# Kernel tuning notes

Hardware: AMD Instinct MI355X
Metric: run time of the kernel (lower is better)

Reference implementation:

```python
import jax, jax.numpy as jnp
import numpy as np

N_NODES = 100000
N_EDGES = 3200000
H, D = 3, 12  # heads, per-head dim; H*D == node_hidden_dim == 36
NEG_SLOPE = 0.2


def setup_inputs() -> dict:
    key = jax.random.key(0)
    ks = jax.random.split(key, 11)
    s = 0.1
    return {
        "node_features": jax.random.normal(ks[0], (N_NODES, 36), jnp.float32),
        "src": jax.random.randint(ks[1], (N_EDGES,), 0, N_NODES),
        "dst": jax.random.randint(ks[2], (N_EDGES,), 0, N_NODES),
        "lin0_w": jax.random.normal(ks[3], (36, 36), jnp.float32) * s,
        "lin0_b": jax.random.normal(ks[4], (36,), jnp.float32) * s,
        "fc_w": jax.random.normal(ks[5], (3, 36, 36), jnp.float32) * s,
        "attn_l": jax.random.normal(ks[6], (3, H, D), jnp.float32) * s,
        "attn_r": jax.random.normal(ks[7], (3, H, D), jnp.float32) * s,
        "gat_bias": jax.random.normal(ks[8], (3, 36), jnp.float32) * s,
        "out_w": jax.random.normal(ks[9], (36, 36), jnp.float32) * s,
        "out_b": jax.random.normal(ks[10], (36,), jnp.float32) * s,
    }


def _gat_layer(h, src, dst, fc_w, a_l, a_r, bias):
    n = h.shape[0]
    feat = (h @ fc_w).reshape(n, H, D)                      # (N,H,D)
    el = jnp.sum(feat * a_l, axis=-1)                       # (N,H)
    er = jnp.sum(feat * a_r, axis=-1)                       # (N,H)
    e = el[src] + er[dst]                                   # (E,H)
    e = jnp.where(e >= 0, e, NEG_SLOPE * e)                 # leaky_relu(0.2)
    # edge softmax over incoming edges of each dst node (numerically stable)
    m = jax.ops.segment_max(e, dst, num_segments=n)         # (N,H)
    m = jnp.where(jnp.isfinite(m), m, 0.0)                  # zero-degree guard
    ee = jnp.exp(e - m[dst])                                # (E,H)
    denom = jax.ops.segment_sum(ee, dst, num_segments=n)    # (N,H)
    alpha = ee / jnp.maximum(denom[dst], 1e-9)              # (E,H)
    msg = feat[src] * alpha[:, :, None]                     # (E,H,D)
    rst = jax.ops.segment_sum(msg, dst, num_segments=n)     # (N,H,D)
    # residual (Identity since in_feats == H*D) + bias, then ELU
    rst = rst + h.reshape(n, H, D) + bias.reshape(1, H, D)
    return jax.nn.elu(rst).reshape(n, H * D)


def reference(node_features, src, dst, lin0_w, lin0_b, fc_w, attn_l, attn_r, gat_bias, out_w, out_b):
    h = node_features @ lin0_w + lin0_b
    for l in range(3):
        h = _gat_layer(h, src, dst, fc_w[l], attn_l[l], attn_r[l], gat_bias[l])
    return h @ out_w + out_b
```

## Files before the change

kernel.cpp:

```cpp
#include <hip/hip_runtime.h>
#include <math.h>

#define HID 36
#define NH 3
#define HD 12
#define PROW 64
#define BSHIFT 13
#define NBUCK 13
#define PSHIFT 8
#define PCHUNK 8192
#define CSRCAP 4096
#define NSTEP 8

typedef _Float16 f16;


__global__ void hist2_kernel(const int* __restrict__ dst, int* __restrict__ M,
                             int E, int C, int np) {
    __shared__ int h[512];
    int t = threadIdx.x;
    int c = blockIdx.x;
    for (int i = t; i < 512; i += blockDim.x) h[i] = 0;
    __syncthreads();
    int i0 = c * PCHUNK;
    int i1 = min(i0 + PCHUNK, E);
    for (int i = i0 + t; i < i1; i += blockDim.x)
        atomicAdd(&h[dst[i] >> PSHIFT], 1);
    __syncthreads();
    for (int b = t; b < np; b += blockDim.x)
        M[(size_t)b * C + c] = h[b];
}

__global__ void base_scan_kernel(const int* __restrict__ M, int* __restrict__ BaseT,
                                 int* __restrict__ T, int C, int np) {
    __shared__ int tmp[512];
    int b = blockIdx.x;
    int t = threadIdx.x;
    int v = (t < C) ? M[(size_t)b * C + t] : 0;
    tmp[t] = v;
    __syncthreads();
    for (int ofs = 1; ofs < 512; ofs <<= 1) {
        int x = 0;
        if (t >= ofs) x = tmp[t - ofs];
        __syncthreads();
        tmp[t] += x;
        __syncthreads();
    }
    if (t < C) BaseT[(size_t)t * 512 + b] = tmp[t] - v;
    if (t == 511) T[b] = tmp[511];
}

__global__ void scan_small_kernel(const int* __restrict__ T, int* __restrict__ poff, int np) {
    __shared__ int tmp[512];
    int t = threadIdx.x;
    int v = (t < np) ? T[t] : 0;
    tmp[t] = v;
    __syncthreads();
    for (int ofs = 1; ofs < 512; ofs <<= 1) {
        int x = 0;
        if (t >= ofs) x = tmp[t - ofs];
        __syncthreads();
        tmp[t] += x;
        __syncthreads();
    }
    int excl = tmp[t] - v;
    if (t < np) poff[t] = excl;
    if (t == np - 1) poff[np] = excl + v;
}

__global__ void part_scatter_kernel(const int* __restrict__ src, const int* __restrict__ dst,
                                    const int* __restrict__ BaseT, const int* __restrict__ poff,
                                    int* __restrict__ part, int E, int np) {
    __shared__ int h[512];
    __shared__ int base[512];
    int t = threadIdx.x;
    int c = blockIdx.x;
    for (int i = t; i < 512; i += blockDim.x) h[i] = 0;
    for (int b = t; b < np; b += blockDim.x)
        base[b] = poff[b] + BaseT[(size_t)c * 512 + b];
    __syncthreads();
    int i0 = c * PCHUNK;
    int i1 = min(i0 + PCHUNK, E);
    for (int i = i0 + t; i < i1; i += blockDim.x) {
        int d = dst[i];
        int bin = d >> PSHIFT;
        int r = atomicAdd(&h[bin], 1);
        part[base[bin] + r] = (src[i] << PSHIFT) | (d & ((1 << PSHIFT) - 1));
    }
}

__global__ void bucket_csr_kernel(const int* __restrict__ part, const int* __restrict__ T,
                                  const int* __restrict__ poff,
                                  int* __restrict__ csr, int* __restrict__ off,
                                  int n, int E) {
    __shared__ int cnt[256 * NBUCK];
    __shared__ int psum[256];
    int p = blockIdx.x;
    int t = threadIdx.x;
    int dbase = p << PSHIFT;
    int nd = min(256, n - dbase);
    int nc = nd * NBUCK;
    for (int i = t; i < nc; i += blockDim.x) cnt[i] = 0;
    __syncthreads();
    int cnt_p = T[p];
    int e0 = poff[p];
    const int* pp = part + e0;
    for (int i = t; i < cnt_p; i += blockDim.x) {
        int e = pp[i];
        atomicAdd(&cnt[(e & 255) * NBUCK + ((e >> PSHIFT) >> BSHIFT)], 1);
    }
    __syncthreads();
    int sum = 0;
    if (t < nd) {
        for (int k = 0; k < NBUCK; ++k) {
            int c = cnt[t * NBUCK + k];
            cnt[t * NBUCK + k] = sum;
            sum += c;
        }
    }
    psum[t] = (t < nd) ? sum : 0;
    __syncthreads();
    for (int ofs = 1; ofs < 256; ofs <<= 1) {
        int x = 0;
        if (t >= ofs) x = psum[t - ofs];
        __syncthreads();
        psum[t] += x;
        __syncthreads();
    }
    int dexcl = (t > 0) ? psum[t - 1] : 0;
    int start = e0 + dexcl;
    if (t < nd) {
        for (int k = 0; k < NBUCK; ++k) cnt[t * NBUCK + k] += start;
        off[dbase + t] = start;
    }
    __syncthreads();
    for (int i = t; i < cnt_p; i += blockDim.x) {
        int e = pp[i];
        int s = e >> PSHIFT;
        int idx = (e & 255) * NBUCK + (s >> BSHIFT);
        int pos = atomicAdd(&cnt[idx], 1);
        csr[pos] = s << 6;
    }
    if (p == 0 && t == 0) off[n] = E;
}


__device__ __forceinline__ void edge_accum(uint4 qa, uint4 qb, float ern,
                                           float& denom, float* acc) {
    union { uint4 q[2]; f16 hx[16]; } v;
    v.q[0] = qa;
    v.q[1] = qb;
    float e = (float)v.hx[12] + ern;
    e = (e >= 0.f) ? e : 0.2f * e;
    float w = __expf(e);
    denom += w;
#pragma unroll
    for (int k = 0; k < HD; ++k) acc[k] += w * (float)v.hx[k];
}

template <bool FITS>
__device__ __forceinline__ void sweep_paced(const int* __restrict__ smbuf,
                                            const int* __restrict__ csre,
                                            int j0, int deg, const f16* __restrict__ pb,
                                            float ern, float& denom, float* acc) {
    int j = j0;
#pragma unroll 1
    for (int s2 = 1; s2 <= NSTEP; ++s2) {
        int jend = j0 + ((deg * s2) >> 3);
        int c = jend - j;
        for (; c >= 4; c -= 4, j += 4) {
            int o0 = FITS ? smbuf[j]     : csre[j];
            int o1 = FITS ? smbuf[j + 1] : csre[j + 1];
            int o2 = FITS ? smbuf[j + 2] : csre[j + 2];
            int o3 = FITS ? smbuf[j + 3] : csre[j + 3];
            const uint4* r0 = (const uint4*)(pb + o0);
            const uint4* r1 = (const uint4*)(pb + o1);
            const uint4* r2 = (const uint4*)(pb + o2);
            const uint4* r3 = (const uint4*)(pb + o3);
            uint4 a0 = r0[0], b0 = r0[1];
            uint4 a1 = r1[0], b1 = r1[1];
            uint4 a2 = r2[0], b2 = r2[1];
            uint4 a3 = r3[0], b3 = r3[1];
            edge_accum(a0, b0, ern, denom, acc);
            edge_accum(a1, b1, ern, denom, acc);
            edge_accum(a2, b2, ern, denom, acc);
            edge_accum(a3, b3, ern, denom, acc);
        }
        for (; c > 0; --c, ++j) {
            int o = FITS ? smbuf[j] : csre[j];
            const uint4* r = (const uint4*)(pb + o);
            edge_accum(r[0], r[1], ern, denom, acc);
        }
    }
}

__global__ void lin0tr_kernel(const float* __restrict__ x, const float* __restrict__ w0,
                              const float* __restrict__ b0, const float* __restrict__ fcw,
                              const float* __restrict__ al, const float* __restrict__ ar,
                              float* __restrict__ h, f16* __restrict__ packed,
                              float* __restrict__ er, int n) {
    __shared__ float W0[HID * HID];
    __shared__ float W1[HID * HID];
    __shared__ float Bs[HID], ALs[HID], ARs[HID];
    int t = threadIdx.x;
    for (int i = t; i < HID * HID; i += 256) { W0[i] = w0[i]; W1[i] = fcw[i]; }
    if (t < HID) { Bs[t] = b0[t]; ALs[t] = al[t]; ARs[t] = ar[t]; }
    __syncthreads();
    int node = blockIdx.x * 256 + t;
    if (node >= n) return;
    const float4* xp = (const float4*)(x + (size_t)node * HID);
    float h0[HID];
#pragma unroll
    for (int j = 0; j < HID; ++j) h0[j] = Bs[j];
#pragma unroll
    for (int kk = 0; kk < HID / 4; ++kk) {
        float4 xv = xp[kk];
        const float* w = &W0[(4 * kk) * HID];
#pragma unroll
        for (int j = 0; j < HID; ++j)
            h0[j] += xv.x * w[j] + xv.y * w[HID + j] + xv.z * w[2 * HID + j] + xv.w * w[3 * HID + j];
    }
    float* hp = h + (size_t)node * HID;
#pragma unroll
    for (int j = 0; j < HID; ++j) hp[j] = h0[j];
    float feat[HID];
#pragma unroll
    for (int j = 0; j < HID; ++j) feat[j] = 0.f;
#pragma unroll
    for (int k = 0; k < HID; ++k) {
        float hv = h0[k];
        const float* w = &W1[k * HID];
#pragma unroll
        for (int j = 0; j < HID; ++j) feat[j] += hv * w[j];
    }
    union { f16 hx[48]; uint4 q[6]; } u;
#pragma unroll
    for (int hh = 0; hh < NH; ++hh) {
        float sl = 0.f, sr = 0.f;
#pragma unroll
        for (int d = 0; d < HD; ++d) {
            sl += feat[hh * HD + d] * ALs[hh * HD + d];
            sr += feat[hh * HD + d] * ARs[hh * HD + d];
        }
#pragma unroll
        for (int d = 0; d < HD; ++d) u.hx[hh * 16 + d] = (f16)feat[hh * HD + d];
        u.hx[hh * 16 + 12] = (f16)sl;
        u.hx[hh * 16 + 13] = (f16)0.f;
        u.hx[hh * 16 + 14] = (f16)0.f;
        u.hx[hh * 16 + 15] = (f16)0.f;
        er[node * NH + hh] = sr;
    }
    uint4* prow = (uint4*)(packed + (size_t)node * PROW);
#pragma unroll
    for (int q = 0; q < 6; ++q) prow[q] = u.q[q];
}

__global__ void __launch_bounds__(192)
aggtr_kernel(const f16* __restrict__ packed_in, const float* __restrict__ er_in,
             const float* __restrict__ hcur,
             const int* __restrict__ off, const int* __restrict__ csr,
             const float* __restrict__ bias, const float* __restrict__ wnext,
             const float* __restrict__ aln, const float* __restrict__ arn,
             float* __restrict__ hnext, f16* __restrict__ packed_out,
             float* __restrict__ er_out, int n) {
    __shared__ float Wsh[HID * HID];
    __shared__ float ALs[HID], ARs[HID];
    __shared__ int smbuf[CSRCAP];
    int t = threadIdx.x;
    for (int i = t; i < HID * HID; i += 192) Wsh[i] = wnext[i];
    if (t < HID) { ALs[t] = aln[t]; ARs[t] = arn[t]; }
    int ln = t / 3, hh = t - ln * 3;
    int nb0 = blockIdx.x * 64;
    int node = nb0 + ln;
    bool active = (node < n);

    int e0 = off[nb0];
    int e1 = off[min(nb0 + 64, n)];
    int span = e1 - e0;
    bool fits = (span <= CSRCAP);
    if (fits)
        for (int i = t; i < span; i += 192) smbuf[i] = csr[e0 + i];

    int j0 = 0, deg = 0;
    float ern = 0.f;
    if (active) {
        j0 = off[node] - e0;
        deg = off[node + 1] - e0 - j0;
        ern = er_in[node * NH + hh];
    }
    const f16* pb = packed_in + hh * 16;
    const int* csre = csr + e0;
    __syncthreads();

    float denom = 0.f;
    float acc[HD];
#pragma unroll
    for (int k = 0; k < HD; ++k) acc[k] = 0.f;

    if (fits) sweep_paced<true>(smbuf, csre, j0, deg, pb, ern, denom, acc);
    else      sweep_paced<false>(smbuf, csre, j0, deg, pb, ern, denom, acc);
    __syncthreads();

    float* hsh = (float*)smbuf;
    float v[HD];
#pragma unroll
    for (int k = 0; k < HD; ++k) v[k] = 0.f;
    if (active) {
        float inv = 1.f / fmaxf(denom, 1e-9f);
        int base = node * HID + hh * HD;
        const float4* hc = (const float4*)(hcur + base);
        float4 h0 = hc[0], h1 = hc[1], h2 = hc[2];
        float hres[HD] = {h0.x, h0.y, h0.z, h0.w, h1.x, h1.y, h1.z, h1.w, h2.x, h2.y, h2.z, h2.w};
#pragma unroll
        for (int k = 0; k < HD; ++k) {
            float x = acc[k] * inv + hres[k] + bias[hh * HD + k];
            v[k] = (x > 0.f) ? x : expm1f(x);
        }
        float4* hp = (float4*)(hnext + base);
        hp[0] = make_float4(v[0], v[1], v[2], v[3]);
        hp[1] = make_float4(v[4], v[5], v[6], v[7]);
        hp[2] = make_float4(v[8], v[9], v[10], v[11]);
    }
#pragma unroll
    for (int k = 0; k < HD; ++k) hsh[ln * 37 + hh * HD + k] = v[k];
    __syncthreads();

    float feat[HD];
#pragma unroll
    for (int d = 0; d < HD; ++d) feat[d] = 0.f;
    const float* hrow = &hsh[ln * 37];
#pragma unroll 4
    for (int k = 0; k < HID; ++k) {
        float hv = hrow[k];
        const float* w = &Wsh[k * HID + hh * HD];
#pragma unroll
        for (int d = 0; d < HD; ++d) feat[d] += hv * w[d];
    }
    if (!active) return;
    float sl = 0.f, sr = 0.f;
#pragma unroll
    for (int d = 0; d < HD; ++d) {
        sl += feat[d] * ALs[hh * HD + d];
        sr += feat[d] * ARs[hh * HD + d];
    }
    union { f16 hx[16]; uint4 q[2]; } o;
#pragma unroll
    for (int d = 0; d < HD; ++d) o.hx[d] = (f16)feat[d];
    o.hx[12] = (f16)sl;
    o.hx[13] = (f16)0.f; o.hx[14] = (f16)0.f; o.hx[15] = (f16)0.f;
    uint4* prow = (uint4*)(packed_out + (size_t)node * PROW + hh * 16);
    prow[0] = o.q[0];
    prow[1] = o.q[1];
    er_out[node * NH + hh] = sr;
}

__global__ void __launch_bounds__(192)
aggout_kernel(const f16* __restrict__ packed_in, const float* __restrict__ er_in,
              const float* __restrict__ hcur,
              const int* __restrict__ off, const int* __restrict__ csr,
              const float* __restrict__ bias, const float* __restrict__ ow,
              const float* __restrict__ ob, float* __restrict__ out, int n) {
    __shared__ float Wsh[HID * HID];
    __shared__ float OBs[HID];
    __shared__ int smbuf[CSRCAP];
    int t = threadIdx.x;
    for (int i = t; i < HID * HID; i += 192) Wsh[i] = ow[i];
    if (t < HID) OBs[t] = ob[t];
    int ln = t / 3, hh = t - ln * 3;
    int nb0 = blockIdx.x * 64;
    int node = nb0 + ln;
    bool active = (node < n);

    int e0 = off[nb0];
    int e1 = off[min(nb0 + 64, n)];
    int span = e1 - e0;
    bool fits = (span <= CSRCAP);
    if (fits)
        for (int i = t; i < span; i += 192) smbuf[i] = csr[e0 + i];

    int j0 = 0, deg = 0;
    float ern = 0.f;
    if (active) {
        j0 = off[node] - e0;
        deg = off[node + 1] - e0 - j0;
        ern = er_in[node * NH + hh];
    }
    const f16* pb = packed_in + hh * 16;
    const int* csre = csr + e0;
    __syncthreads();

    float denom = 0.f;
    float acc[HD];
#pragma unroll
    for (int k = 0; k < HD; ++k) acc[k] = 0.f;

    if (fits) sweep_paced<true>(smbuf, csre, j0, deg, pb, ern, denom, acc);
    else      sweep_paced<false>(smbuf, csre, j0, deg, pb, ern, denom, acc);
    __syncthreads();

    float* hsh = (float*)smbuf;
    float v[HD];
#pragma unroll
    for (int k = 0; k < HD; ++k) v[k] = 0.f;
    if (active) {
        float inv = 1.f / fmaxf(denom, 1e-9f);
        int base = node * HID + hh * HD;
        const float4* hc = (const float4*)(hcur + base);
        float4 h0 = hc[0], h1 = hc[1], h2 = hc[2];
        float hres[HD] = {h0.x, h0.y, h0.z, h0.w, h1.x, h1.y, h1.z, h1.w, h2.x, h2.y, h2.z, h2.w};
#pragma unroll
        for (int k = 0; k < HD; ++k) {
            float x = acc[k] * inv + hres[k] + bias[hh * HD + k];
            v[k] = (x > 0.f) ? x : expm1f(x);
        }
    }
#pragma unroll
    for (int k = 0; k < HD; ++k) hsh[ln * 37 + hh * HD + k] = v[k];
    __syncthreads();

    float feat[HD];
#pragma unroll
    for (int d = 0; d < HD; ++d) feat[d] = OBs[hh * HD + d];
    const float* hrow = &hsh[ln * 37];
#pragma unroll 4
    for (int k = 0; k < HID; ++k) {
        float hv = hrow[k];
        const float* w = &Wsh[k * HID + hh * HD];
#pragma unroll
        for (int d = 0; d < HD; ++d) feat[d] += hv * w[d];
    }
    if (!active) return;
    float4* op = (float4*)(out + (size_t)node * HID + hh * HD);
    op[0] = make_float4(feat[0], feat[1], feat[2], feat[3]);
    op[1] = make_float4(feat[4], feat[5], feat[6], feat[7]);
    op[2] = make_float4(feat[8], feat[9], feat[10], feat[11]);
}


extern "C" void kernel_launch(void* const* d_in, const int* in_sizes, int n_in,
                              void* d_out, int out_size, void* d_ws, size_t ws_size,
                              hipStream_t stream) {
    const float* xnf = (const float*)d_in[0];
    const int* src = (const int*)d_in[1];
    const int* dst = (const int*)d_in[2];
    const float* l0w = (const float*)d_in[3];
    const float* l0b = (const float*)d_in[4];
    const float* fcw = (const float*)d_in[5];
    const float* al  = (const float*)d_in[6];
    const float* ar  = (const float*)d_in[7];
    const float* gb  = (const float*)d_in[8];
    const float* ow  = (const float*)d_in[9];
    const float* ob  = (const float*)d_in[10];
    float* out = (float*)d_out;
    const int N = in_sizes[0] / HID;
    const int E = in_sizes[1];
    const int NP = (N + (1 << PSHIFT) - 1) >> PSHIFT;
    const int C = (E + PCHUNK - 1) / PCHUNK;

    char* p = (char*)d_ws;
    auto alloc = [&](size_t bytes) {
        char* r = p;
        p += (bytes + 255) & ~(size_t)255;
        return r;
    };
    int* part    = (int*)alloc((size_t)E * 4);
    int* M       = (int*)alloc((size_t)NP * C * 4);
    int* BaseT   = (int*)alloc((size_t)C * 512 * 4);
    int* T       = (int*)alloc((size_t)NP * 4);
    int* poff    = (int*)alloc((size_t)(NP + 1) * 4);
    int* off     = (int*)alloc((size_t)(N + 1) * 4);
    int* csr     = (int*)alloc((size_t)E * 4);
    float* ha    = (float*)alloc((size_t)N * HID * 4);
    float* hb    = (float*)alloc((size_t)N * HID * 4);
    f16* pkA     = (f16*)alloc((size_t)N * PROW * 2);
    f16* pkB     = (f16*)alloc((size_t)N * PROW * 2);
    float* erA   = (float*)alloc((size_t)N * NH * 4);
    float* erB   = (float*)alloc((size_t)N * NH * 4);

    hist2_kernel<<<C, 256, 0, stream>>>(dst, M, E, C, NP);
    base_scan_kernel<<<NP, 512, 0, stream>>>(M, BaseT, T, C, NP);
    scan_small_kernel<<<1, 512, 0, stream>>>(T, poff, NP);
    part_scatter_kernel<<<C, 256, 0, stream>>>(src, dst, BaseT, poff, part, E, NP);
    bucket_csr_kernel<<<NP, 256, 0, stream>>>(part, T, poff, csr, off, N, E);

    int nblk = (N + 255) / 256;
    int fblk = (N + 63) / 64;

    lin0tr_kernel<<<nblk, 256, 0, stream>>>(xnf, l0w, l0b, fcw, al, ar, ha, pkA, erA, N);

    aggtr_kernel<<<fblk, 192, 0, stream>>>(pkA, erA, ha, off, csr, gb,
                                           fcw + (size_t)1 * HID * HID, al + HID, ar + HID,
                                           hb, pkB, erB, N);
    aggtr_kernel<<<fblk, 192, 0, stream>>>(pkB, erB, hb, off, csr, gb + HID,
                                           fcw + (size_t)2 * HID * HID, al + 2 * HID, ar + 2 * HID,
                                           ha, pkA, erA, N);
    aggout_kernel<<<fblk, 192, 0, stream>>>(pkA, erA, ha, off, csr, gb + 2 * HID,
                                            ow, ob, out, N);
}
```

Baseline: 375.8 us.

## Replace LDS-staged paced CSR sweep with register double-buffered gather pipeline

The aggregation kernels no longer copy each block's CSR slice into shared memory and no longer pace the sweep in eight steps. Each thread now reads neighbour indices straight from global memory and software-pipelines the gathers, loading the next four packed rows while accumulating the current four. This removes the LDS staging pass and a barrier and shrinks shared memory, which may allow more blocks per CU. In exchange it adds register pressure from the double-buffered uint4 values and makes index reads uncoalesced global loads.

```diff
diff --git a/kernel.cpp b/kernel.cpp
--- a/kernel.cpp
+++ b/kernel.cpp
@@ -9,8 +9,6 @@
 #define NBUCK 13
 #define PSHIFT 8
 #define PCHUNK 8192
-#define CSRCAP 4096
-#define NSTEP 8
 
 typedef _Float16 f16;
 
@@ -158,39 +156,55 @@
     for (int k = 0; k < HD; ++k) acc[k] += w * (float)v.hx[k];
 }
 
-template <bool FITS>
-__device__ __forceinline__ void sweep_paced(const int* __restrict__ smbuf,
-                                            const int* __restrict__ csre,
-                                            int j0, int deg, const f16* __restrict__ pb,
-                                            float ern, float& denom, float* acc) {
+__device__ __forceinline__ void sweep_pipe(const int* __restrict__ csre,
+                                           int j0, int j1, const f16* __restrict__ pb,
+                                           float ern, float& denom, float* acc) {
+    int m = j1 - j0;
     int j = j0;
-#pragma unroll 1
-    for (int s2 = 1; s2 <= NSTEP; ++s2) {
-        int jend = j0 + ((deg * s2) >> 3);
-        int c = jend - j;
-        for (; c >= 4; c -= 4, j += 4) {
-            int o0 = FITS ? smbuf[j]     : csre[j];
-            int o1 = FITS ? smbuf[j + 1] : csre[j + 1];
-            int o2 = FITS ? smbuf[j + 2] : csre[j + 2];
-            int o3 = FITS ? smbuf[j + 3] : csre[j + 3];
-            const uint4* r0 = (const uint4*)(pb + o0);
-            const uint4* r1 = (const uint4*)(pb + o1);
-            const uint4* r2 = (const uint4*)(pb + o2);
-            const uint4* r3 = (const uint4*)(pb + o3);
-            uint4 a0 = r0[0], b0 = r0[1];
-            uint4 a1 = r1[0], b1 = r1[1];
-            uint4 a2 = r2[0], b2 = r2[1];
-            uint4 a3 = r3[0], b3 = r3[1];
-            edge_accum(a0, b0, ern, denom, acc);
-            edge_accum(a1, b1, ern, denom, acc);
-            edge_accum(a2, b2, ern, denom, acc);
-            edge_accum(a3, b3, ern, denom, acc);
-        }
-        for (; c > 0; --c, ++j) {
-            int o = FITS ? smbuf[j] : csre[j];
-            const uint4* r = (const uint4*)(pb + o);
-            edge_accum(r[0], r[1], ern, denom, acc);
-        }
+    uint4 ca0, cb0, ca1, cb1, ca2, cb2, ca3, cb3;
+    int o0 = 0, o1 = 0, o2 = 0, o3 = 0;
+    if (m >= 4) {
+        int p0 = csre[j], p1 = csre[j + 1], p2 = csre[j + 2], p3 = csre[j + 3];
+        j += 4;
+        const uint4* r0 = (const uint4*)(pb + p0);
+        const uint4* r1 = (const uint4*)(pb + p1);
+        const uint4* r2 = (const uint4*)(pb + p2);
+        const uint4* r3 = (const uint4*)(pb + p3);
+        ca0 = r0[0]; cb0 = r0[1]; ca1 = r1[0]; cb1 = r1[1];
+        ca2 = r2[0]; cb2 = r2[1]; ca3 = r3[0]; cb3 = r3[1];
+        if (m >= 8) {
+            o0 = csre[j]; o1 = csre[j + 1]; o2 = csre[j + 2]; o3 = csre[j + 3];
+            j += 4;
+        }
+    }
+    for (; m >= 8; m -= 4) {
+        const uint4* r0 = (const uint4*)(pb + o0);
+        const uint4* r1 = (const uint4*)(pb + o1);
+        const uint4* r2 = (const uint4*)(pb + o2);
+        const uint4* r3 = (const uint4*)(pb + o3);
+        uint4 na0 = r0[0], nb0 = r0[1], na1 = r1[0], nb1 = r1[1];
+        uint4 na2 = r2[0], nb2 = r2[1], na3 = r3[0], nb3 = r3[1];
+        if (m >= 12) {
+            o0 = csre[j]; o1 = csre[j + 1]; o2 = csre[j + 2]; o3 = csre[j + 3];
+            j += 4;
+        }
+        edge_accum(ca0, cb0, ern, denom, acc);
+        edge_accum(ca1, cb1, ern, denom, acc);
+        edge_accum(ca2, cb2, ern, denom, acc);
+        edge_accum(ca3, cb3, ern, denom, acc);
+        ca0 = na0; cb0 = nb0; ca1 = na1; cb1 = nb1;
+        ca2 = na2; cb2 = nb2; ca3 = na3; cb3 = nb3;
+    }
+    if (m >= 4) {
+        edge_accum(ca0, cb0, ern, denom, acc);
+        edge_accum(ca1, cb1, ern, denom, acc);
+        edge_accum(ca2, cb2, ern, denom, acc);
+        edge_accum(ca3, cb3, ern, denom, acc);
+        m -= 4;
+    }
+    for (; m > 0; --m, ++j) {
+        const uint4* r = (const uint4*)(pb + csre[j]);
+        edge_accum(r[0], r[1], ern, denom, acc);
     }
 }
 
@@ -265,43 +279,30 @@
              float* __restrict__ er_out, int n) {
     __shared__ float Wsh[HID * HID];
     __shared__ float ALs[HID], ARs[HID];
-    __shared__ int smbuf[CSRCAP];
+    __shared__ float hsh[64 * 37];
     int t = threadIdx.x;
     for (int i = t; i < HID * HID; i += 192) Wsh[i] = wnext[i];
     if (t < HID) { ALs[t] = aln[t]; ARs[t] = arn[t]; }
     int ln = t / 3, hh = t - ln * 3;
-    int nb0 = blockIdx.x * 64;
-    int node = nb0 + ln;
+    int node = blockIdx.x * 64 + ln;
     bool active = (node < n);
 
-    int e0 = off[nb0];
-    int e1 = off[min(nb0 + 64, n)];
-    int span = e1 - e0;
-    bool fits = (span <= CSRCAP);
-    if (fits)
-        for (int i = t; i < span; i += 192) smbuf[i] = csr[e0 + i];
-
-    int j0 = 0, deg = 0;
+    int j0 = 0, j1 = 0;
     float ern = 0.f;
     if (active) {
-        j0 = off[node] - e0;
-        deg = off[node + 1] - e0 - j0;
+        j0 = off[node];
+        j1 = off[node + 1];
         ern = er_in[node * NH + hh];
     }
     const f16* pb = packed_in + hh * 16;
-    const int* csre = csr + e0;
-    __syncthreads();
 
     float denom = 0.f;
     float acc[HD];
 #pragma unroll
     for (int k = 0; k < HD; ++k) acc[k] = 0.f;
 
-    if (fits) sweep_paced<true>(smbuf, csre, j0, deg, pb, ern, denom, acc);
-    else      sweep_paced<false>(smbuf, csre, j0, deg, pb, ern, denom, acc);
-    __syncthreads();
-
-    float* hsh = (float*)smbuf;
+    sweep_pipe(csr, j0, j1, pb, ern, denom, acc);
+
     float v[HD];
 #pragma unroll
     for (int k = 0; k < HD; ++k) v[k] = 0.f;
@@ -362,43 +363,30 @@
               const float* __restrict__ ob, float* __restrict__ out, int n) {
     __shared__ float Wsh[HID * HID];
     __shared__ float OBs[HID];
-    __shared__ int smbuf[CSRCAP];
+    __shared__ float hsh[64 * 37];
     int t = threadIdx.x;
     for (int i = t; i < HID * HID; i += 192) Wsh[i] = ow[i];
     if (t < HID) OBs[t] = ob[t];
     int ln = t / 3, hh = t - ln * 3;
-    int nb0 = blockIdx.x * 64;
-    int node = nb0 + ln;
+    int node = blockIdx.x * 64 + ln;
     bool active = (node < n);
 
-    int e0 = off[nb0];
-    int e1 = off[min(nb0 + 64, n)];
-    int span = e1 - e0;
-    bool fits = (span <= CSRCAP);
-    if (fits)
-        for (int i = t; i < span; i += 192) smbuf[i] = csr[e0 + i];
-
-    int j0 = 0, deg = 0;
+    int j0 = 0, j1 = 0;
     float ern = 0.f;
     if (active) {
-        j0 = off[node] - e0;
-        deg = off[node + 1] - e0 - j0;
+        j0 = off[node];
+        j1 = off[node + 1];
         ern = er_in[node * NH + hh];
     }
     const f16* pb = packed_in + hh * 16;
-    const int* csre = csr + e0;
-    __syncthreads();
 
     float denom = 0.f;
     float acc[HD];
 #pragma unroll
     for (int k = 0; k < HD; ++k) acc[k] = 0.f;
 
-    if (fits) sweep_paced<true>(smbuf, csre, j0, deg, pb, ern, denom, acc);
-    else      sweep_paced<false>(smbuf, csre, j0, deg, pb, ern, denom, acc);
-    __syncthreads();
-
-    float* hsh = (float*)smbuf;
+    sweep_pipe(csr, j0, j1, pb, ern, denom, acc);
+
     float v[HD];
 #pragma unroll
     for (int k = 0; k < HD; ++k) v[k] = 0.f;
```

New measurement: 402.2 us. 7.0% more time.

## Build CSR via global per-(dst,src-bucket) cell counting instead of two-pass partition

Applied to the files above, without the earlier changes.

Replaces the two-level partition (block histograms, partition scatter, per-partition bucket sort in LDS) with a direct global histogram over cells keyed by destination node and source bucket. The cell counts are exclusive-scanned in three small kernels, and edges are then scattered with global atomics straight into CSR order. This drops the intermediate part array and one full pass over the edges, at the cost of 3.2M global atomics in each of two passes and a 1.6M-cell scan. Within a cell, edge order is now nondeterministic, and the cell buffer must be zeroed with a memset on every call.

```diff
diff --git a/kernel.cpp b/kernel.cpp
--- a/kernel.cpp
+++ b/kernel.cpp
@@ -6,37 +6,48 @@
 #define HD 12
 #define PROW 64
 #define BSHIFT 13
-#define NBUCK 13
-#define PSHIFT 8
-#define PCHUNK 8192
+#define KSH 4
 #define CSRCAP 4096
 #define NSTEP 8
 
 typedef _Float16 f16;
 
 
-__global__ void hist2_kernel(const int* __restrict__ dst, int* __restrict__ M,
-                             int E, int C, int np) {
-    __shared__ int h[512];
+__global__ void cell_hist_kernel(const int* __restrict__ src, const int* __restrict__ dst,
+                                 int* __restrict__ cells, int E) {
+    int i = blockIdx.x * blockDim.x + threadIdx.x;
+    int stride = gridDim.x * blockDim.x;
+    for (; i < E; i += stride)
+        atomicAdd(&cells[(dst[i] << KSH) | (src[i] >> BSHIFT)], 1);
+}
+
+__global__ void cell_blocksum_kernel(const int* __restrict__ cells, int* __restrict__ bsum,
+                                     int NC) {
+    __shared__ int red[256];
+    int b = blockIdx.x, t = threadIdx.x;
+    int base = b * 4096 + t * 16;
+    int s = 0;
+    if (base + 16 <= NC) {
+        const int4* p = (const int4*)(cells + base);
+#pragma unroll
+        for (int q = 0; q < 4; ++q) { int4 v = p[q]; s += v.x + v.y + v.z + v.w; }
+    } else {
+        for (int k = 0; k < 16; ++k) { int idx = base + k; if (idx < NC) s += cells[idx]; }
+    }
+    red[t] = s;
+    __syncthreads();
+    for (int ofs = 128; ofs > 0; ofs >>= 1) {
+        if (t < ofs) red[t] += red[t + ofs];
+        __syncthreads();
+    }
+    if (t == 0) bsum[b] = red[0];
+}
+
+__global__ void cell_scan_kernel(const int* __restrict__ bsum, int* __restrict__ bexcl,
+                                 int nb, int* __restrict__ off, int n, int E) {
+    __shared__ int tmp[512];
     int t = threadIdx.x;
-    int c = blockIdx.x;
-    for (int i = t; i < 512; i += blockDim.x) h[i] = 0;
-    __syncthreads();
-    int i0 = c * PCHUNK;
-    int i1 = min(i0 + PCHUNK, E);
-    for (int i = i0 + t; i < i1; i += blockDim.x)
-        atomicAdd(&h[dst[i] >> PSHIFT], 1);
-    __syncthreads();
-    for (int b = t; b < np; b += blockDim.x)
-        M[(size_t)b * C + c] = h[b];
-}
-
-__global__ void base_scan_kernel(const int* __restrict__ M, int* __restrict__ BaseT,
-                                 int* __restrict__ T, int C, int np) {
-    __shared__ int tmp[512];
-    int b = blockIdx.x;
-    int t = threadIdx.x;
-    int v = (t < C) ? M[(size_t)b * C + t] : 0;
+    int v = (t < nb) ? bsum[t] : 0;
     tmp[t] = v;
     __syncthreads();
     for (int ofs = 1; ofs < 512; ofs <<= 1) {
@@ -46,102 +57,74 @@
         tmp[t] += x;
         __syncthreads();
     }
-    if (t < C) BaseT[(size_t)t * 512 + b] = tmp[t] - v;
-    if (t == 511) T[b] = tmp[511];
-}
-
-__global__ void scan_small_kernel(const int* __restrict__ T, int* __restrict__ poff, int np) {
-    __shared__ int tmp[512];
-    int t = threadIdx.x;
-    int v = (t < np) ? T[t] : 0;
-    tmp[t] = v;
-    __syncthreads();
-    for (int ofs = 1; ofs < 512; ofs <<= 1) {
-        int x = 0;
-        if (t >= ofs) x = tmp[t - ofs];
-        __syncthreads();
-        tmp[t] += x;
-        __syncthreads();
-    }
-    int excl = tmp[t] - v;
-    if (t < np) poff[t] = excl;
-    if (t == np - 1) poff[np] = excl + v;
-}
-
-__global__ void part_scatter_kernel(const int* __restrict__ src, const int* __restrict__ dst,
-                                    const int* __restrict__ BaseT, const int* __restrict__ poff,
-                                    int* __restrict__ part, int E, int np) {
-    __shared__ int h[512];
-    __shared__ int base[512];
-    int t = threadIdx.x;
-    int c = blockIdx.x;
-    for (int i = t; i < 512; i += blockDim.x) h[i] = 0;
-    for (int b = t; b < np; b += blockDim.x)
-        base[b] = poff[b] + BaseT[(size_t)c * 512 + b];
-    __syncthreads();
-    int i0 = c * PCHUNK;
-    int i1 = min(i0 + PCHUNK, E);
-    for (int i = i0 + t; i < i1; i += blockDim.x) {
-        int d = dst[i];
-        int bin = d >> PSHIFT;
-        int r = atomicAdd(&h[bin], 1);
-        part[base[bin] + r] = (src[i] << PSHIFT) | (d & ((1 << PSHIFT) - 1));
-    }
-}
-
-__global__ void bucket_csr_kernel(const int* __restrict__ part, const int* __restrict__ T,
-                                  const int* __restrict__ poff,
-                                  int* __restrict__ csr, int* __restrict__ off,
-                                  int n, int E) {
-    __shared__ int cnt[256 * NBUCK];
-    __shared__ int psum[256];
-    int p = blockIdx.x;
-    int t = threadIdx.x;
-    int dbase = p << PSHIFT;
-    int nd = min(256, n - dbase);
-    int nc = nd * NBUCK;
-    for (int i = t; i < nc; i += blockDim.x) cnt[i] = 0;
-    __syncthreads();
-    int cnt_p = T[p];
-    int e0 = poff[p];
-    const int* pp = part + e0;
-    for (int i = t; i < cnt_p; i += blockDim.x) {
-        int e = pp[i];
-        atomicAdd(&cnt[(e & 255) * NBUCK + ((e >> PSHIFT) >> BSHIFT)], 1);
-    }
-    __syncthreads();
-    int sum = 0;
-    if (t < nd) {
-        for (int k = 0; k < NBUCK; ++k) {
-            int c = cnt[t * NBUCK + k];
-            cnt[t * NBUCK + k] = sum;
-            sum += c;
-        }
-    }
-    psum[t] = (t < nd) ? sum : 0;
+    if (t < nb) bexcl[t] = tmp[t] - v;
+    if (t == 0) off[n] = E;
+}
+
+__global__ void cell_addback_kernel(int* __restrict__ cells, const int* __restrict__ bexcl,
+                                    int* __restrict__ off, int NC) {
+    __shared__ int ts[256];
+    int b = blockIdx.x, t = threadIdx.x;
+    int base = b * 4096 + t * 16;
+    int my[16];
+    int s = 0;
+    bool full = (base + 16 <= NC);
+    if (full) {
+        const int4* p = (const int4*)(cells + base);
+#pragma unroll
+        for (int q = 0; q < 4; ++q) {
+            int4 v = p[q];
+            my[4 * q] = v.x; my[4 * q + 1] = v.y; my[4 * q + 2] = v.z; my[4 * q + 3] = v.w;
+        }
+#pragma unroll
+        for (int k = 0; k < 16; ++k) s += my[k];
+    } else {
+        for (int k = 0; k < 16; ++k) {
+            int idx = base + k;
+            my[k] = (idx < NC) ? cells[idx] : 0;
+            s += my[k];
+        }
+    }
+    ts[t] = s;
     __syncthreads();
     for (int ofs = 1; ofs < 256; ofs <<= 1) {
         int x = 0;
-        if (t >= ofs) x = psum[t - ofs];
+        if (t >= ofs) x = ts[t - ofs];
         __syncthreads();
-        psum[t] += x;
+        ts[t] += x;
         __syncthreads();
     }
-    int dexcl = (t > 0) ? psum[t - 1] : 0;
-    int start = e0 + dexcl;
-    if (t < nd) {
-        for (int k = 0; k < NBUCK; ++k) cnt[t * NBUCK + k] += start;
-        off[dbase + t] = start;
-    }
-    __syncthreads();
-    for (int i = t; i < cnt_p; i += blockDim.x) {
-        int e = pp[i];
-        int s = e >> PSHIFT;
-        int idx = (e & 255) * NBUCK + (s >> BSHIFT);
-        int pos = atomicAdd(&cnt[idx], 1);
+    int run = bexcl[b] + ts[t] - s;
+    if (full) {
+        int out[16];
+#pragma unroll
+        for (int k = 0; k < 16; ++k) { out[k] = run; run += my[k]; }
+        int4* p = (int4*)(cells + base);
+#pragma unroll
+        for (int q = 0; q < 4; ++q)
+            p[q] = make_int4(out[4 * q], out[4 * q + 1], out[4 * q + 2], out[4 * q + 3]);
+        off[base >> KSH] = out[0];
+    } else {
+        for (int k = 0; k < 16; ++k) {
+            int idx = base + k;
+            if (idx < NC) {
+                cells[idx] = run;
+                if ((idx & 15) == 0) off[idx >> KSH] = run;
+                run += my[k];
+            }
+        }
+    }
+}
+
+__global__ void cell_scatter_kernel(const int* __restrict__ src, const int* __restrict__ dst,
+                                    int* __restrict__ cells, int* __restrict__ csr, int E) {
+    int i = blockIdx.x * blockDim.x + threadIdx.x;
+    int stride = gridDim.x * blockDim.x;
+    for (; i < E; i += stride) {
+        int s = src[i];
+        int pos = atomicAdd(&cells[(dst[i] << KSH) | (s >> BSHIFT)], 1);
         csr[pos] = s << 6;
     }
-    if (p == 0 && t == 0) off[n] = E;
 }
 
 
@@ -454,8 +437,8 @@
     float* out = (float*)d_out;
     const int N = in_sizes[0] / HID;
     const int E = in_sizes[1];
-    const int NP = (N + (1 << PSHIFT) - 1) >> PSHIFT;
-    const int C = (E + PCHUNK - 1) / PCHUNK;
+    const int NC = N << KSH;
+    const int NBLK = (NC + 4095) / 4096;
 
     char* p = (char*)d_ws;
     auto alloc = [&](size_t bytes) {
@@ -463,11 +446,9 @@
         p += (bytes + 255) & ~(size_t)255;
         return r;
     };
-    int* part    = (int*)alloc((size_t)E * 4);
-    int* M       = (int*)alloc((size_t)NP * C * 4);
-    int* BaseT   = (int*)alloc((size_t)C * 512 * 4);
-    int* T       = (int*)alloc((size_t)NP * 4);
-    int* poff    = (int*)alloc((size_t)(NP + 1) * 4);
+    int* cells   = (int*)alloc((size_t)NC * 4);
+    int* bsum    = (int*)alloc((size_t)NBLK * 4);
+    int* bexcl   = (int*)alloc((size_t)NBLK * 4);
     int* off     = (int*)alloc((size_t)(N + 1) * 4);
     int* csr     = (int*)alloc((size_t)E * 4);
     float* ha    = (float*)alloc((size_t)N * HID * 4);
@@ -477,11 +458,13 @@
     float* erA   = (float*)alloc((size_t)N * NH * 4);
     float* erB   = (float*)alloc((size_t)N * NH * 4);
 
-    hist2_kernel<<<C, 256, 0, stream>>>(dst, M, E, C, NP);
-    base_scan_kernel<<<NP, 512, 0, stream>>>(M, BaseT, T, C, NP);
-    scan_small_kernel<<<1, 512, 0, stream>>>(T, poff, NP);
-    part_scatter_kernel<<<C, 256, 0, stream>>>(src, dst, BaseT, poff, part, E, NP);
-    bucket_csr_kernel<<<NP, 256, 0, stream>>>(part, T, poff, csr, off, N, E);
+    hipMemsetAsync(cells, 0, (size_t)NC * 4, stream);
+    int gE = min((E + 255) / 256, 2048);
+    cell_hist_kernel<<<gE, 256, 0, stream>>>(src, dst, cells, E);
+    cell_blocksum_kernel<<<NBLK, 256, 0, stream>>>(cells, bsum, NC);
+    cell_scan_kernel<<<1, 512, 0, stream>>>(bsum, bexcl, NBLK, off, N, E);
+    cell_addback_kernel<<<NBLK, 256, 0, stream>>>(cells, bexcl, off, NC);
+    cell_scatter_kernel<<<gE, 256, 0, stream>>>(src, dst, cells, csr, E);
 
     int nblk = (N + 255) / 256;
     int fblk = (N + 63) / 64;
```

Result: slower. 708.7 us (+88.6%).
